# Kernel optimization log

Hardware: AMD Instinct MI355X
Metric: run time of the kernel (lower is better)

## Reference

```python
import jax, jax.numpy as jnp
import numpy as np

K = 4  # hard-coded in ParticleNet.__init__

# (fan_in, fan_out) for all linear layers
_DIMS = [(10, 32), (32, 64),        # edgeconv1 MLP (2*5 -> 32 -> 64)
         (128, 96), (96, 128),      # edgeconv2 MLP (2*64 -> 96 -> 128)
         (256, 192), (192, 256),    # edgeconv3 MLP (2*128 -> 192 -> 256)
         (453, 453), (453, 226), (226, 2)]  # output head (5+64+128+256=453)
_PNAMES = ['c1w1', 'c1w2', 'c2w1', 'c2w2', 'c3w1', 'c3w2', 'ow1', 'ow2', 'ow3']


def setup_inputs() -> dict:
    key = jax.random.key(0)
    ks = jax.random.split(key, 2 + len(_DIMS))
    inp = {
        'coords': jax.random.normal(ks[0], (1024, 128, 2), dtype=jnp.float32),
        'features': jax.random.normal(ks[1], (1024, 128, 5), dtype=jnp.float32),
    }
    for i, (name, (fi, fo)) in enumerate(zip(_PNAMES, _DIMS)):
        inp[name] = jax.random.normal(ks[2 + i], (fi, fo), dtype=jnp.float32) / np.sqrt(fi)
        inp[name.replace('w', 'b')] = jnp.zeros((fo,), dtype=jnp.float32)
    return inp


def _knn_idx(x, k):
    # x: [B,N,C] -> idx of k nearest neighbors (excluding self): [B,N,k]
    x2 = jnp.sum(x * x, axis=-1)                              # [B,N]
    d = x2[:, :, None] + x2[:, None, :] - 2.0 * jnp.einsum('bnc,bmc->bnm', x, x)
    d = d + jnp.eye(x.shape[1], dtype=x.dtype) * 1e9          # no self-loops
    _, idx = jax.lax.top_k(-d, k)
    return idx


def _edgeconv(x, idx, w1, b1, w2, b2):
    # EdgeConv: message = MLP([x_i, x_j - x_i]), mean-aggregated over k neighbors
    xj = jax.vmap(lambda xb, ib: xb[ib])(x, idx)              # [B,N,k,C]
    xi = jnp.broadcast_to(x[:, :, None, :], xj.shape)
    h = jnp.concatenate([xi, xj - xi], axis=-1)               # [B,N,k,2C]
    h = jax.nn.elu(h @ w1 + b1)
    h = jax.nn.elu(h @ w2 + b2)
    return jnp.mean(h, axis=2)                                # [B,N,out]


def reference(coords, features, c1w1, c1b1, c1w2, c1b2, c2w1, c2b1, c2w2, c2b2,
              c3w1, c3b1, c3w2, c3b2, ow1, ob1, ow2, ob2, ow3, ob3):
    idx1 = _knn_idx(coords, K)
    out1 = _edgeconv(features, idx1, c1w1, c1b1, c1w2, c1b2)  # [B,N,64]
    idx2 = _knn_idx(out1, K)
    out2 = _edgeconv(out1, idx2, c2w1, c2b1, c2w2, c2b2)      # [B,N,128]
    idx3 = _knn_idx(out2, K)
    out3 = _edgeconv(out2, idx3, c3w1, c3b1, c3w2, c3b2)      # [B,N,256]
    h = jnp.concatenate([features, out1, out2, out3], axis=-1)  # [B,N,453]
    h = jax.nn.elu(h @ ow1 + ob1)
    h = jax.nn.elu(h @ ow2 + ob2)
    return h @ ow3 + ob3                                      # [B,N,2]
```

## Files before the change

### kernel.cpp

```cpp
#include <hip/hip_runtime.h>
#include <cstdint>
#include <cstddef>


#define NB 1024
#define NPT 128

typedef __attribute__((ext_vector_type(8))) short short8;
typedef __attribute__((ext_vector_type(4))) float floatx4;
typedef __attribute__((ext_vector_type(4))) unsigned int uint4v;

__device__ __forceinline__ float elu_f(float x) { return x > 0.0f ? x : expm1f(x); }

__device__ __forceinline__ unsigned short f2bf(float f) {
  unsigned u = __builtin_bit_cast(unsigned, f);
  unsigned r = u + 0x7FFFu + ((u >> 16) & 1u);
  return (unsigned short)(r >> 16);
}
__device__ __forceinline__ float bf2f(unsigned short h) {
  unsigned u = ((unsigned)h) << 16;
  return __builtin_bit_cast(float, u);
}

template<int C>
__global__ __launch_bounds__(128) void knn_kernel(const float* __restrict__ x,
                                                  int* __restrict__ idx) {
  __shared__ __align__(16) float xs[NPT][C + 4];
  __shared__ float x2s[NPT];
  __shared__ double x2d[NPT];
  const int b = blockIdx.x, t = threadIdx.x;
  const float* xb = x + (size_t)b * NPT * C;
  for (int e = t; e < NPT * C; e += 128) xs[e / C][e % C] = xb[e];
  __syncthreads();
  float xi[C];
  float s2 = 0.0f;
  double s2d = 0.0;
#pragma unroll
  for (int c = 0; c < C; ++c) {
    xi[c] = xs[t][c];
    s2 += xi[c] * xi[c];
    s2d += (double)xi[c] * (double)xi[c];
  }
  x2s[t] = s2;
  x2d[t] = s2d;
  __syncthreads();
  float bd0 = 1e30f, bd1 = 1e30f, bd2 = 1e30f, bd3 = 1e30f, bd4 = 1e30f, bd5 = 1e30f;
  int bi0 = 0, bi1 = 0, bi2 = 0, bi3 = 0, bi4 = 0, bi5 = 0;
  for (int j = 0; j < NPT; ++j) {
    if (j == t) continue;
    float dot = 0.0f;
#pragma unroll
    for (int c = 0; c < C; ++c) dot += xi[c] * xs[j][c];
    float d = s2 + x2s[j] - 2.0f * dot;
    if (d < bd5) {
      bd5 = d; bi5 = j;
      if (bd5 < bd4) {
        float td = bd4; bd4 = bd5; bd5 = td; int ti = bi4; bi4 = bi5; bi5 = ti;
        if (bd4 < bd3) {
          td = bd3; bd3 = bd4; bd4 = td; ti = bi3; bi3 = bi4; bi4 = ti;
          if (bd3 < bd2) {
            td = bd2; bd2 = bd3; bd3 = td; ti = bi2; bi2 = bi3; bi3 = ti;
            if (bd2 < bd1) {
              td = bd1; bd1 = bd2; bd2 = td; ti = bi1; bi1 = bi2; bi2 = ti;
              if (bd1 < bd0) {
                td = bd0; bd0 = bd1; bd1 = td; ti = bi0; bi0 = bi1; bi1 = ti;
              }
            }
          }
        }
      }
    }
  }
  auto refine = [&](int j) -> double {
    double dot = 0.0;
#pragma unroll
    for (int c = 0; c < C; ++c) dot += (double)xi[c] * (double)xs[j][c];
    return s2d + x2d[j] - 2.0 * dot;
  };
  double e0 = refine(bi0), e1 = refine(bi1), e2 = refine(bi2);
  double e3 = refine(bi3), e4 = refine(bi4), e5 = refine(bi5);
#define CSWP(da, ia, db, ib)                                            \
  if ((da > db) || (da == db && ia > ib)) {                             \
    double _td = da; da = db; db = _td; int _ti = ia; ia = ib; ib = _ti; }
  CSWP(e0, bi0, e1, bi1) CSWP(e1, bi1, e2, bi2) CSWP(e2, bi2, e3, bi3)
  CSWP(e3, bi3, e4, bi4) CSWP(e4, bi4, e5, bi5)
  CSWP(e0, bi0, e1, bi1) CSWP(e1, bi1, e2, bi2) CSWP(e2, bi2, e3, bi3)
  CSWP(e3, bi3, e4, bi4)
  CSWP(e0, bi0, e1, bi1) CSWP(e1, bi1, e2, bi2) CSWP(e2, bi2, e3, bi3)
  CSWP(e0, bi0, e1, bi1) CSWP(e1, bi1, e2, bi2)
  CSWP(e0, bi0, e1, bi1)
#undef CSWP
  int* ib = idx + ((size_t)b * NPT + t) * 4;
  ib[0] = bi0; ib[1] = bi1; ib[2] = bi2; ib[3] = bi3;
}

template<int C>
__global__ __launch_bounds__(512) void knn512_kernel(const float* __restrict__ x,
                                                     int* __restrict__ idx) {
  constexpr int CQ = C / 4;
  constexpr int QS = CQ + 4;
  __shared__ __align__(16) float xs[NPT][4 * QS];
  __shared__ float x2s[NPT];
  __shared__ double x2d[NPT];
  const int b = blockIdx.x, t = threadIdx.x;
  const float* xb = x + (size_t)b * NPT * C;
  for (int e = t; e < NPT * C; e += 512) {
    int r = e / C, c = e % C;
    xs[r][(c / CQ) * QS + (c % CQ)] = xb[e];
  }
  __syncthreads();
  const int p = t >> 2, q = t & 3;
  float xi[CQ];
  float s2 = 0.f;
  double s2d = 0.0;
#pragma unroll
  for (int c = 0; c < CQ; ++c) {
    xi[c] = xs[p][q * QS + c];
    s2 += xi[c] * xi[c];
    s2d += (double)xi[c] * (double)xi[c];
  }
  s2 += __shfl_xor(s2, 1);  s2 += __shfl_xor(s2, 2);
  s2d += __shfl_xor(s2d, 1); s2d += __shfl_xor(s2d, 2);
  if (q == 0) { x2s[p] = s2; x2d[p] = s2d; }
  __syncthreads();
  float bd0 = 1e30f, bd1 = 1e30f, bd2 = 1e30f, bd3 = 1e30f, bd4 = 1e30f, bd5 = 1e30f;
  int bi0 = 0, bi1 = 0, bi2 = 0, bi3 = 0, bi4 = 0, bi5 = 0;
  for (int j = 0; j < NPT; ++j) {
    if (j == p) continue;
    const float4* xr = reinterpret_cast<const float4*>(&xs[j][q * QS]);
    float part0 = 0.f, part1 = 0.f, part2 = 0.f, part3 = 0.f;
#pragma unroll
    for (int c4 = 0; c4 < CQ / 4; ++c4) {
      float4 v = xr[c4];
      float s = xi[4 * c4 + 0] * v.x + xi[4 * c4 + 1] * v.y +
                xi[4 * c4 + 2] * v.z + xi[4 * c4 + 3] * v.w;
      if ((c4 & 3) == 0) part0 += s;
      else if ((c4 & 3) == 1) part1 += s;
      else if ((c4 & 3) == 2) part2 += s;
      else part3 += s;
    }
    float dot = (part0 + part1) + (part2 + part3);
    dot += __shfl_xor(dot, 1);
    dot += __shfl_xor(dot, 2);
    float d = s2 + x2s[j] - 2.0f * dot;
    if (d < bd5) {
      bd5 = d; bi5 = j;
      if (bd5 < bd4) {
        float td = bd4; bd4 = bd5; bd5 = td; int ti = bi4; bi4 = bi5; bi5 = ti;
        if (bd4 < bd3) {
          td = bd3; bd3 = bd4; bd4 = td; ti = bi3; bi3 = bi4; bi4 = ti;
          if (bd3 < bd2) {
            td = bd2; bd2 = bd3; bd3 = td; ti = bi2; bi2 = bi3; bi3 = ti;
            if (bd2 < bd1) {
              td = bd1; bd1 = bd2; bd2 = td; ti = bi1; bi1 = bi2; bi2 = ti;
              if (bd1 < bd0) {
                td = bd0; bd0 = bd1; bd1 = td; ti = bi0; bi0 = bi1; bi1 = ti;
              }
            }
          }
        }
      }
    }
  }
  auto refine = [&](int j) -> double {
    double dot = 0.0;
#pragma unroll
    for (int c = 0; c < CQ; ++c) dot += (double)xi[c] * (double)xs[j][q * QS + c];
    dot += __shfl_xor(dot, 1);
    dot += __shfl_xor(dot, 2);
    return s2d + x2d[j] - 2.0 * dot;
  };
  double e0 = refine(bi0), e1 = refine(bi1), e2 = refine(bi2);
  double e3 = refine(bi3), e4 = refine(bi4), e5 = refine(bi5);
#define CSWP(da, ia, db, ib)                                            \
  if ((da > db) || (da == db && ia > ib)) {                             \
    double _td = da; da = db; db = _td; int _ti = ia; ia = ib; ib = _ti; }
  CSWP(e0, bi0, e1, bi1) CSWP(e1, bi1, e2, bi2) CSWP(e2, bi2, e3, bi3)
  CSWP(e3, bi3, e4, bi4) CSWP(e4, bi4, e5, bi5)
  CSWP(e0, bi0, e1, bi1) CSWP(e1, bi1, e2, bi2) CSWP(e2, bi2, e3, bi3)
  CSWP(e3, bi3, e4, bi4)
  CSWP(e0, bi0, e1, bi1) CSWP(e1, bi1, e2, bi2) CSWP(e2, bi2, e3, bi3)
  CSWP(e0, bi0, e1, bi1) CSWP(e1, bi1, e2, bi2)
  CSWP(e0, bi0, e1, bi1)
#undef CSWP
  if (q == 0) {
    int* ib = idx + ((size_t)b * NPT + p) * 4;
    ib[0] = bi0; ib[1] = bi1; ib[2] = bi2; ib[3] = bi3;
  }
}

__global__ __launch_bounds__(256) void ec1_kernel(
    const float* __restrict__ feat, const int* __restrict__ idx,
    const float* __restrict__ w1, const float* __restrict__ b1,
    const float* __restrict__ w2, const float* __restrict__ b2,
    float* __restrict__ out) {
  __shared__ __align__(16) float fs[NPT][6];
  __shared__ __align__(16) float w1s[10][32];
  __shared__ __align__(16) float w2s[32][68];
  __shared__ float hs[256][33];
  __shared__ float b1s[32], b2s[64];
  const int z = blockIdx.x, t = threadIdx.x;
  const int b = z >> 1, hh = z & 1;
  const float* fb = feat + (size_t)b * NPT * 5;
  for (int e = t; e < NPT * 5; e += 256) fs[e / 5][e % 5] = fb[e];
  for (int e = t; e < 320; e += 256) w1s[e / 32][e % 32] = w1[e];
  for (int e = t; e < 2048; e += 256) w2s[e >> 6][e & 63] = w2[e];
  if (t < 32) b1s[t] = b1[t];
  if (t >= 192) b2s[t - 192] = b2[t - 192];
  __syncthreads();
  {
    const int p = hh * 64 + (t >> 2);
    const int j = idx[(size_t)b * 512 + p * 4 + (t & 3)];
    float h[32];
#pragma unroll
    for (int o = 0; o < 32; ++o) h[o] = b1s[o];
#pragma unroll
    for (int c = 0; c < 10; ++c) {
      float in_c = (c < 5) ? fs[p][c] : (fs[j][c - 5] - fs[p][c - 5]);
      const float4* wr = reinterpret_cast<const float4*>(&w1s[c][0]);
#pragma unroll
      for (int o4 = 0; o4 < 8; ++o4) {
        float4 w = wr[o4];
        h[4 * o4 + 0] += in_c * w.x; h[4 * o4 + 1] += in_c * w.y;
        h[4 * o4 + 2] += in_c * w.z; h[4 * o4 + 3] += in_c * w.w;
      }
    }
#pragma unroll
    for (int o = 0; o < 32; ++o) hs[t][o] = elu_f(h[o]);
  }
  __syncthreads();
  {
    const int g = t >> 2, q = t & 3;
    const int o0 = q * 16;
    float acc[4][16];
#pragma unroll
    for (int m = 0; m < 16; ++m) {
      float bv = b2s[o0 + m];
#pragma unroll
      for (int i = 0; i < 4; ++i) acc[i][m] = bv;
    }
    for (int k = 0; k < 32; ++k) {
      float hk0 = hs[g * 4 + 0][k];
      float hk1 = hs[g * 4 + 1][k];
      float hk2 = hs[g * 4 + 2][k];
      float hk3 = hs[g * 4 + 3][k];
      const float4* wr = reinterpret_cast<const float4*>(&w2s[k][o0]);
#pragma unroll
      for (int m4 = 0; m4 < 4; ++m4) {
        float4 w = wr[m4];
        acc[0][4 * m4 + 0] += hk0 * w.x; acc[0][4 * m4 + 1] += hk0 * w.y;
        acc[0][4 * m4 + 2] += hk0 * w.z; acc[0][4 * m4 + 3] += hk0 * w.w;
        acc[1][4 * m4 + 0] += hk1 * w.x; acc[1][4 * m4 + 1] += hk1 * w.y;
        acc[1][4 * m4 + 2] += hk1 * w.z; acc[1][4 * m4 + 3] += hk1 * w.w;
        acc[2][4 * m4 + 0] += hk2 * w.x; acc[2][4 * m4 + 1] += hk2 * w.y;
        acc[2][4 * m4 + 2] += hk2 * w.z; acc[2][4 * m4 + 3] += hk2 * w.w;
        acc[3][4 * m4 + 0] += hk3 * w.x; acc[3][4 * m4 + 1] += hk3 * w.y;
        acc[3][4 * m4 + 2] += hk3 * w.z; acc[3][4 * m4 + 3] += hk3 * w.w;
      }
    }
    float* ob = out + ((size_t)b * NPT + hh * 64 + g) * 64 + o0;
#pragma unroll
    for (int m4 = 0; m4 < 4; ++m4) {
      float4 v;
      float* vp = &v.x;
#pragma unroll
      for (int s = 0; s < 4; ++s) {
        int m = 4 * m4 + s;
        vp[s] = 0.25f * (elu_f(acc[0][m]) + elu_f(acc[1][m]) +
                         elu_f(acc[2][m]) + elu_f(acc[3][m]));
      }
      *reinterpret_cast<float4*>(&ob[4 * m4]) = v;
    }
  }
}

__global__ __launch_bounds__(512, 2) void ec2a_kernel(
    const float* __restrict__ x, const int* __restrict__ idx,
    const float* __restrict__ w1, const float* __restrict__ b1,
    float* __restrict__ H) {
  __shared__ __align__(16) float xs[NPT][68];
  __shared__ __align__(16) float w1s[128][100];
  __shared__ float b1s[96];
  const int b = blockIdx.x, t = threadIdx.x;
  const float* xb = x + (size_t)b * NPT * 64;
  for (int e = t; e < NPT * 64; e += 512) xs[e >> 6][e & 63] = xb[e];
  for (int e = t; e < 128 * 96; e += 512) w1s[e / 96][e % 96] = w1[e];
  if (t < 96) b1s[t] = b1[t];
  __syncthreads();
  const int pb = t >> 2, part = t & 3;
  const int n0 = part * 24;
  int jn[4];
#pragma unroll
  for (int i = 0; i < 4; ++i) jn[i] = idx[(size_t)b * 512 + pb * 4 + i];
  float acc[4][24];
#pragma unroll
  for (int m = 0; m < 24; ++m) {
    float bv = b1s[n0 + m];
#pragma unroll
    for (int i = 0; i < 4; ++i) acc[i][m] = bv;
  }
  for (int c = 0; c < 64; ++c) {
    float in_c = xs[pb][c];
    const float4* wr = reinterpret_cast<const float4*>(&w1s[c][n0]);
#pragma unroll
    for (int q4 = 0; q4 < 6; ++q4) {
      float4 wv = wr[q4];
#pragma unroll
      for (int i = 0; i < 4; ++i) {
        acc[i][4 * q4 + 0] += in_c * wv.x;
        acc[i][4 * q4 + 1] += in_c * wv.y;
        acc[i][4 * q4 + 2] += in_c * wv.z;
        acc[i][4 * q4 + 3] += in_c * wv.w;
      }
    }
  }
  for (int c = 0; c < 64; ++c) {
    float xic = xs[pb][c];
    float in0 = xs[jn[0]][c] - xic;
    float in1 = xs[jn[1]][c] - xic;
    float in2 = xs[jn[2]][c] - xic;
    float in3 = xs[jn[3]][c] - xic;
    const float4* wr = reinterpret_cast<const float4*>(&w1s[64 + c][n0]);
#pragma unroll
    for (int q4 = 0; q4 < 6; ++q4) {
      float4 wv = wr[q4];
      acc[0][4 * q4 + 0] += in0 * wv.x; acc[0][4 * q4 + 1] += in0 * wv.y;
      acc[0][4 * q4 + 2] += in0 * wv.z; acc[0][4 * q4 + 3] += in0 * wv.w;
      acc[1][4 * q4 + 0] += in1 * wv.x; acc[1][4 * q4 + 1] += in1 * wv.y;
      acc[1][4 * q4 + 2] += in1 * wv.z; acc[1][4 * q4 + 3] += in1 * wv.w;
      acc[2][4 * q4 + 0] += in2 * wv.x; acc[2][4 * q4 + 1] += in2 * wv.y;
      acc[2][4 * q4 + 2] += in2 * wv.z; acc[2][4 * q4 + 3] += in2 * wv.w;
      acc[3][4 * q4 + 0] += in3 * wv.x; acc[3][4 * q4 + 1] += in3 * wv.y;
      acc[3][4 * q4 + 2] += in3 * wv.z; acc[3][4 * q4 + 3] += in3 * wv.w;
    }
  }
#pragma unroll
  for (int i = 0; i < 4; ++i) {
    float* hrow = H + ((size_t)b * 512 + pb * 4 + i) * 96 + n0;
#pragma unroll
    for (int q4 = 0; q4 < 6; ++q4) {
      float4 v = {elu_f(acc[i][4 * q4 + 0]), elu_f(acc[i][4 * q4 + 1]),
                  elu_f(acc[i][4 * q4 + 2]), elu_f(acc[i][4 * q4 + 3])};
      *reinterpret_cast<float4*>(&hrow[4 * q4]) = v;
    }
  }
}

__global__ __launch_bounds__(512, 2) void ec2b_kernel(
    const float* __restrict__ H, const float* __restrict__ w2,
    const float* __restrict__ b2, float* __restrict__ out) {
  __shared__ __align__(16) float hsT[96][260];
  __shared__ float w2s[96][132];
  __shared__ float b2s[128];
  const int z = blockIdx.x, t = threadIdx.x;
  const int bc = z >> 1, hh = z & 1;
  const float* Hb = H + ((size_t)bc * 512 + hh * 256) * 96;
  for (int i = t; i < 256 * 96; i += 512) hsT[i % 96][i / 96] = Hb[i];
  for (int i = t; i < 96 * 128; i += 512) w2s[i >> 7][i & 127] = w2[i];
  if (t < 128) b2s[t] = b2[t];
  __syncthreads();
  const int g = t >> 3, oq = t & 7;
  float acc[4][16];
#pragma unroll
  for (int m = 0; m < 16; ++m) {
    float bv = b2s[oq + 8 * m];
#pragma unroll
    for (int i = 0; i < 4; ++i) acc[i][m] = bv;
  }
  for (int k = 0; k < 96; ++k) {
    float4 hv = *reinterpret_cast<const float4*>(&hsT[k][4 * g]);
#pragma unroll
    for (int m = 0; m < 16; ++m) {
      float wv = w2s[k][oq + 8 * m];
      acc[0][m] += hv.x * wv;
      acc[1][m] += hv.y * wv;
      acc[2][m] += hv.z * wv;
      acc[3][m] += hv.w * wv;
    }
  }
  float* orow = out + ((size_t)bc * NPT + hh * 64 + g) * 128;
#pragma unroll
  for (int m = 0; m < 16; ++m) {
    float s = elu_f(acc[0][m]) + elu_f(acc[1][m]) +
              elu_f(acc[2][m]) + elu_f(acc[3][m]);
    orow[oq + 8 * m] = 0.25f * s;
  }
}

__global__ __launch_bounds__(512, 2) void ec3a_kernel(
    const float* __restrict__ x, const int* __restrict__ idx,
    const float* __restrict__ w1, const float* __restrict__ b1,
    unsigned short* __restrict__ h1) {
  __shared__ unsigned short Xb[128][136];
  __shared__ unsigned short W1t[192][264];
  __shared__ float b1s[192];
  __shared__ unsigned short stg[8][16][40];
  const int b = blockIdx.x, t = threadIdx.x;
  const float* xb = x + (size_t)b * NPT * 128;
  for (int e = t; e < NPT * 128; e += 512) Xb[e >> 7][e & 127] = f2bf(xb[e]);
  for (int e = t; e < 256 * 192; e += 512) {
    int k = e / 192, n = e % 192;
    W1t[n][k] = f2bf(w1[e]);
  }
  if (t < 192) b1s[t] = b1[t];
  __syncthreads();
  const int w = t >> 6, l = t & 63;
  const int lr = l & 15, lq = l >> 4;
  for (int mt = 0; mt < 4; ++mt) {
    const int m = (w * 4 + mt) * 16;
    const int e = m + lr;
    const int p = e >> 2;
    const int jp = idx[(size_t)b * 512 + e];
    short8 A[8];
#pragma unroll
    for (int kk = 0; kk < 4; ++kk) {
      int k0 = kk * 32 + lq * 8;
      A[kk] = *reinterpret_cast<const short8*>(&Xb[p][k0]);
    }
#pragma unroll
    for (int kk = 0; kk < 4; ++kk) {
      int k0 = kk * 32 + lq * 8;
      short8 aj = *reinterpret_cast<const short8*>(&Xb[jp][k0]);
      short8 ai = *reinterpret_cast<const short8*>(&Xb[p][k0]);
      short8 d;
#pragma unroll
      for (int q = 0; q < 8; ++q)
        d[q] = (short)f2bf(bf2f((unsigned short)aj[q]) - bf2f((unsigned short)ai[q]));
      A[4 + kk] = d;
    }
    floatx4 acc[12];
#pragma unroll
    for (int n = 0; n < 12; ++n) acc[n] = (floatx4){0.f, 0.f, 0.f, 0.f};
#pragma unroll
    for (int n = 0; n < 12; ++n) {
#pragma unroll
      for (int kk = 0; kk < 8; ++kk) {
        short8 Bf = *reinterpret_cast<const short8*>(&W1t[n * 16 + lr][kk * 32 + lq * 8]);
        acc[n] = __builtin_amdgcn_mfma_f32_16x16x32_bf16(A[kk], Bf, acc[n], 0, 0, 0);
      }
    }
#pragma unroll
    for (int pr = 0; pr < 6; ++pr) {
      float bv0 = b1s[pr * 32 + lr];
      float bv1 = b1s[pr * 32 + 16 + lr];
#pragma unroll
      for (int i = 0; i < 4; ++i) {
        stg[w][lq * 4 + i][lr]      = f2bf(elu_f(acc[2 * pr][i] + bv0));
        stg[w][lq * 4 + i][16 + lr] = f2bf(elu_f(acc[2 * pr + 1][i] + bv1));
      }
      asm volatile("s_waitcnt lgkmcnt(0)" ::: "memory");
      const unsigned short* src = &stg[w][l >> 2][(l & 3) * 8];
      uint4v vv = *reinterpret_cast<const uint4v*>(src);
      size_t dst = ((size_t)b * 512 + m + (l >> 2)) * 192 + pr * 32 + (l & 3) * 8;
      *reinterpret_cast<uint4v*>(&h1[dst]) = vv;
      asm volatile("s_waitcnt lgkmcnt(0)" ::: "memory");
    }
  }
}

__global__ __launch_bounds__(512, 2) void ec3b_kernel(
    const unsigned short* __restrict__ h1,
    const float* __restrict__ w2, const float* __restrict__ b2,
    unsigned short* __restrict__ out3) {
  __shared__ unsigned short W2t[256][200];
  __shared__ float b2s[256];
  const int b = blockIdx.x, t = threadIdx.x;
  for (int e = t; e < 192 * 256; e += 512) {
    int k = e >> 8, n = e & 255;
    W2t[n][k] = f2bf(w2[e]);
  }
  if (t < 256) b2s[t] = b2[t];
  __syncthreads();
  const int w = t >> 6, l = t & 63;
  const int lr = l & 15, lq = l >> 4;
  for (int mt = 0; mt < 4; ++mt) {
    const int m = (w * 4 + mt) * 16;
    floatx4 acc[16];
#pragma unroll
    for (int n = 0; n < 16; ++n) acc[n] = (floatx4){0.f, 0.f, 0.f, 0.f};
    const unsigned short* arow = h1 + ((size_t)b * 512 + m + lr) * 192;
#pragma unroll
    for (int kk = 0; kk < 6; ++kk) {
      short8 Af = *reinterpret_cast<const short8*>(&arow[kk * 32 + lq * 8]);
#pragma unroll
      for (int n = 0; n < 16; ++n) {
        short8 Bf = *reinterpret_cast<const short8*>(&W2t[n * 16 + lr][kk * 32 + lq * 8]);
        acc[n] = __builtin_amdgcn_mfma_f32_16x16x32_bf16(Af, Bf, acc[n], 0, 0, 0);
      }
    }
    unsigned short* orow = out3 + ((size_t)b * NPT + (m >> 2) + lq) * 256;
#pragma unroll
    for (int n = 0; n < 16; ++n) {
      float bv = b2s[n * 16 + lr];
      float s = 0.f;
#pragma unroll
      for (int i = 0; i < 4; ++i) s += elu_f(acc[n][i] + bv);
      orow[n * 16 + lr] = f2bf(0.25f * s);
    }
  }
}

__global__ __launch_bounds__(256) void head_prep_kernel(
    const float* __restrict__ w1, const float* __restrict__ w2,
    unsigned short* __restrict__ w1p, unsigned short* __restrict__ w2p) {
  int i = blockIdx.x * 256 + threadIdx.x;
  if (i < 512 * 480) {
    int n = i / 480, kp = i % 480;
    int ko = (kp < 5) ? kp : kp - 3;
    bool ok = ((kp < 5) || (kp >= 8 && kp < 456)) && (n < 453);
    w1p[i] = ok ? f2bf(w1[(size_t)ko * 453 + n]) : (unsigned short)0;
  } else {
    int j = i - 512 * 480;
    if (j < 256 * 480) {
      int n = j / 480, kp = j % 480;
      bool ok = (kp < 453) && (n < 226);
      w2p[j] = ok ? f2bf(w2[(size_t)kp * 226 + n]) : (unsigned short)0;
    }
  }
}

#define HSTR 488
#define TPSS 72
__global__ __launch_bounds__(256, 2) void head_mfma_kernel(
    const float* __restrict__ feat, const float* __restrict__ o1,
    const float* __restrict__ o2, const unsigned short* __restrict__ o3,
    const unsigned short* __restrict__ w1p, const float* __restrict__ b1,
    const unsigned short* __restrict__ w2p, const float* __restrict__ b2,
    const float* __restrict__ w3, const float* __restrict__ b3,
    float* __restrict__ out) {
  __shared__ unsigned short uA[64 * HSTR];
  __shared__ __align__(16) unsigned short tps[4][16][TPSS];
  __shared__ float b1s[512], b2s[256], w3s[512];
  const int t = threadIdx.x;
  const size_t base = (size_t)blockIdx.x * 64;

  for (int e = t; e < 64 * 8; e += 256) {
    int r = e >> 3, c = e & 7;
    uA[r * HSTR + c] = (c < 5) ? f2bf(feat[(base + r) * 5 + c]) : 0;
  }
  for (int e = t; e < 64 * 64; e += 256) {
    int r = e >> 6, c = e & 63;
    uA[r * HSTR + 8 + c] = f2bf(o1[(base + r) * 64 + c]);
  }
  for (int e = t; e < 64 * 128; e += 256) {
    int r = e >> 7, c = e & 127;
    uA[r * HSTR + 72 + c] = f2bf(o2[(base + r) * 128 + c]);
  }
  for (int e = t; e < 64 * 256; e += 256) {
    int r = e >> 8, c = e & 255;
    uA[r * HSTR + 200 + c] = o3[(base + r) * 256 + c];
  }
  for (int e = t; e < 64 * 32; e += 256) {
    int r = e >> 5, c = e & 31;
    uA[r * HSTR + 456 + c] = 0;
  }
  for (int i = t; i < 512; i += 256) b1s[i] = (i < 453) ? b1[i] : 0.f;
  if (t < 256) b2s[t] = (t < 226) ? b2[t] : 0.f;
  for (int i = t; i < 512; i += 256) w3s[i] = (i < 452) ? w3[i] : 0.f;
  __syncthreads();

  const int w = t >> 6, l = t & 63;
  const int lr = l & 15, lq = l >> 4;
  const int tr = t >> 2, tc = t & 3;

  short8 Af[15];
#pragma unroll
  for (int kk = 0; kk < 15; ++kk)
    Af[kk] = *reinterpret_cast<const short8*>(
        &uA[(w * 16 + lr) * HSTR + kk * 32 + lq * 8]);
  __syncthreads();

  uint4v v[15];
#define WLOAD(SRC, CH)                                                   \
  {                                                                      \
    _Pragma("unroll")                                                    \
    for (int i = 0; i < 15; ++i)                                         \
      v[i] = *reinterpret_cast<const uint4v*>(                           \
          &SRC[((size_t)((CH) * 64 + tr)) * 480 + (tc + 4 * i) * 8]);    \
  }
#define WWRITE()                                                         \
  {                                                                      \
    _Pragma("unroll")                                                    \
    for (int i = 0; i < 15; ++i)                                         \
      *reinterpret_cast<uint4v*>(&uA[tr * HSTR + (tc + 4 * i) * 8]) = v[i]; \
  }

  WLOAD(w1p, 0)
  WWRITE()
  __syncthreads();

  short8 Af2[15];
#pragma unroll
  for (int ch = 0; ch < 8; ++ch) {
    if (ch < 7) WLOAD(w1p, ch + 1)
    else       WLOAD(w2p, 0)
    floatx4 a0 = {0.f, 0.f, 0.f, 0.f}, a1 = {0.f, 0.f, 0.f, 0.f};
    floatx4 a2 = {0.f, 0.f, 0.f, 0.f}, a3 = {0.f, 0.f, 0.f, 0.f};
#pragma unroll
    for (int kk = 0; kk < 15; ++kk) {
      int ko = kk * 32 + lq * 8;
      short8 B0 = *reinterpret_cast<const short8*>(&uA[(lr)*HSTR + ko]);
      short8 B1 = *reinterpret_cast<const short8*>(&uA[(16 + lr) * HSTR + ko]);
      short8 B2 = *reinterpret_cast<const short8*>(&uA[(32 + lr) * HSTR + ko]);
      short8 B3 = *reinterpret_cast<const short8*>(&uA[(48 + lr) * HSTR + ko]);
      a0 = __builtin_amdgcn_mfma_f32_16x16x32_bf16(Af[kk], B0, a0, 0, 0, 0);
      a1 = __builtin_amdgcn_mfma_f32_16x16x32_bf16(Af[kk], B1, a1, 0, 0, 0);
      a2 = __builtin_amdgcn_mfma_f32_16x16x32_bf16(Af[kk], B2, a2, 0, 0, 0);
      a3 = __builtin_amdgcn_mfma_f32_16x16x32_bf16(Af[kk], B3, a3, 0, 0, 0);
    }
    {
      floatx4 aj[4] = {a0, a1, a2, a3};
#pragma unroll
      for (int jx = 0; jx < 4; ++jx) {
        int c = ch * 64 + jx * 16 + lr;
        float bb = b1s[c];
#pragma unroll
        for (int i = 0; i < 4; ++i)
          tps[w][lq * 4 + i][jx * 16 + lr] = f2bf(elu_f(aj[jx][i] + bb));
      }
    }
    asm volatile("s_waitcnt lgkmcnt(0)" ::: "memory");
    Af2[2 * ch] = *reinterpret_cast<const short8*>(&tps[w][lr][lq * 8]);
    if (ch < 7)
      Af2[2 * ch + 1] = *reinterpret_cast<const short8*>(&tps[w][lr][32 + lq * 8]);
    asm volatile("s_waitcnt lgkmcnt(0)" ::: "memory");
    __syncthreads();
    WWRITE()
    __syncthreads();
  }

  float p0[4] = {0.f, 0.f, 0.f, 0.f}, p1[4] = {0.f, 0.f, 0.f, 0.f};
#pragma unroll
  for (int ch = 0; ch < 4; ++ch) {
    if (ch < 3) WLOAD(w2p, ch + 1)
    floatx4 a0 = {0.f, 0.f, 0.f, 0.f}, a1 = {0.f, 0.f, 0.f, 0.f};
    floatx4 a2 = {0.f, 0.f, 0.f, 0.f}, a3 = {0.f, 0.f, 0.f, 0.f};
#pragma unroll
    for (int kk = 0; kk < 15; ++kk) {
      int ko = kk * 32 + lq * 8;
      short8 B0 = *reinterpret_cast<const short8*>(&uA[(lr)*HSTR + ko]);
      short8 B1 = *reinterpret_cast<const short8*>(&uA[(16 + lr) * HSTR + ko]);
      short8 B2 = *reinterpret_cast<const short8*>(&uA[(32 + lr) * HSTR + ko]);
      short8 B3 = *reinterpret_cast<const short8*>(&uA[(48 + lr) * HSTR + ko]);
      a0 = __builtin_amdgcn_mfma_f32_16x16x32_bf16(Af2[kk], B0, a0, 0, 0, 0);
      a1 = __builtin_amdgcn_mfma_f32_16x16x32_bf16(Af2[kk], B1, a1, 0, 0, 0);
      a2 = __builtin_amdgcn_mfma_f32_16x16x32_bf16(Af2[kk], B2, a2, 0, 0, 0);
      a3 = __builtin_amdgcn_mfma_f32_16x16x32_bf16(Af2[kk], B3, a3, 0, 0, 0);
    }
    {
      floatx4 aj[4] = {a0, a1, a2, a3};
#pragma unroll
      for (int jx = 0; jx < 4; ++jx) {
        int c = ch * 64 + jx * 16 + lr;
        float bb = b2s[c];
        float wa = w3s[2 * c], wb = w3s[2 * c + 1];
#pragma unroll
        for (int i = 0; i < 4; ++i) {
          float h = (c < 226) ? elu_f(aj[jx][i] + bb) : 0.f;
          p0[i] += h * wa;
          p1[i] += h * wb;
        }
      }
    }
    if (ch < 3) {
      __syncthreads();
      WWRITE()
      __syncthreads();
    }
  }

#pragma unroll
  for (int i = 0; i < 4; ++i) {
    float a = p0[i], bvv = p1[i];
#pragma unroll
    for (int m = 1; m < 16; m <<= 1) {
      a += __shfl_xor(a, m);
      bvv += __shfl_xor(bvv, m);
    }
    if (lr == 0) {
      size_t row = base + w * 16 + lq * 4 + i;
      float2 vv = {a + b3[0], bvv + b3[1]};
      *reinterpret_cast<float2*>(&out[row * 2]) = vv;
    }
  }
#undef WLOAD
#undef WWRITE
}

extern "C" void kernel_launch(void* const* d_in, const int* in_sizes, int n_in,
                              void* d_out, int out_size, void* d_ws, size_t ws_size,
                              hipStream_t stream) {
  const float* coords = (const float*)d_in[0];
  const float* feat   = (const float*)d_in[1];
  const float* c1w1 = (const float*)d_in[2];  const float* c1b1 = (const float*)d_in[3];
  const float* c1w2 = (const float*)d_in[4];  const float* c1b2 = (const float*)d_in[5];
  const float* c2w1 = (const float*)d_in[6];  const float* c2b1 = (const float*)d_in[7];
  const float* c2w2 = (const float*)d_in[8];  const float* c2b2 = (const float*)d_in[9];
  const float* c3w1 = (const float*)d_in[10]; const float* c3b1 = (const float*)d_in[11];
  const float* c3w2 = (const float*)d_in[12]; const float* c3b2 = (const float*)d_in[13];
  const float* ow1  = (const float*)d_in[14]; const float* ob1  = (const float*)d_in[15];
  const float* ow2  = (const float*)d_in[16]; const float* ob2  = (const float*)d_in[17];
  const float* ow3  = (const float*)d_in[18]; const float* ob3  = (const float*)d_in[19];
  float* out = (float*)d_out;

  char* ws = (char*)d_ws;
  float* out1 = (float*)(ws);
  float* out2 = (float*)(ws + (32ull << 20));
  unsigned short* out3b = (unsigned short*)(ws + (96ull << 20));
  int* idx = (int*)(ws + (160ull << 20));
  float* Hbuf = (float*)(ws + (162ull << 20));
  unsigned short* h1 = (unsigned short*)(ws + (162ull << 20));
  unsigned short* w1p = (unsigned short*)(ws + (212ull << 20));
  unsigned short* w2p = (unsigned short*)(ws + (213ull << 20));

  head_prep_kernel<<<1440, 256, 0, stream>>>(ow1, ow2, w1p, w2p);
  knn_kernel<2><<<NB, 128, 0, stream>>>(coords, idx);
  ec1_kernel<<<2 * NB, 256, 0, stream>>>(feat, idx, c1w1, c1b1, c1w2, c1b2, out1);
  knn512_kernel<64><<<NB, 512, 0, stream>>>(out1, idx);
  for (int c = 0; c < 4; ++c) {
    ec2a_kernel<<<256, 512, 0, stream>>>(out1 + (size_t)c * 256 * NPT * 64,
                                         idx + (size_t)c * 256 * 512,
                                         c2w1, c2b1, Hbuf);
    ec2b_kernel<<<512, 512, 0, stream>>>(Hbuf, c2w2, c2b2,
                                         out2 + (size_t)c * 256 * NPT * 128);
  }
  knn512_kernel<128><<<NB, 512, 0, stream>>>(out2, idx);
  for (int c = 0; c < 4; ++c) {
    ec3a_kernel<<<256, 512, 0, stream>>>(out2 + (size_t)c * 256 * NPT * 128,
                                         idx + (size_t)c * 256 * 512,
                                         c3w1, c3b1, h1);
    ec3b_kernel<<<256, 512, 0, stream>>>(h1, c3w2, c3b2,
                                         out3b + (size_t)c * 256 * NPT * 256);
  }
  head_mfma_kernel<<<2048, 256, 0, stream>>>(feat, out1, out2, out3b,
                                             w1p, ob1, w2p, ob2, ow3, ob3, out);
}
```

Measured before the change: 2.002 ms.

## Pretranspose ec3 weights once, load head inputs directly, enlarge ec2 chunks

The ec3 layer weights are now converted to bf16 and transposed once in a combined prep kernel. The ec3a/ec3b blocks then copy them into shared memory with vectorized 16-byte loads, instead of each block doing a strided scalar transpose and conversion. The head kernel now loads its A fragments straight from global memory into registers, skipping shared-memory staging and two barriers. ec2 runs in 2 chunks of 512 batches rather than 4, using a larger Hbuf region that aliases the out3 buffer. This aliasing is safe only if ec2 finishes before ec3 writes out3. The change adds workspace relayout and loads the head's global data with less coalescing.

```diff
diff --git a/kernel.cpp b/kernel.cpp
--- a/kernel.cpp
+++ b/kernel.cpp
@@ -389,18 +389,19 @@
 
 __global__ __launch_bounds__(512, 2) void ec3a_kernel(
     const float* __restrict__ x, const int* __restrict__ idx,
-    const float* __restrict__ w1, const float* __restrict__ b1,
+    const unsigned short* __restrict__ w1t3g, const float* __restrict__ b1,
     unsigned short* __restrict__ h1) {
   __shared__ unsigned short Xb[128][136];
-  __shared__ unsigned short W1t[192][264];
+  __shared__ __align__(16) unsigned short W1t[192][264];
   __shared__ float b1s[192];
   __shared__ unsigned short stg[8][16][40];
   const int b = blockIdx.x, t = threadIdx.x;
   const float* xb = x + (size_t)b * NPT * 128;
   for (int e = t; e < NPT * 128; e += 512) Xb[e >> 7][e & 127] = f2bf(xb[e]);
-  for (int e = t; e < 256 * 192; e += 512) {
-    int k = e / 192, n = e % 192;
-    W1t[n][k] = f2bf(w1[e]);
+  {
+    const uint4v* src = reinterpret_cast<const uint4v*>(w1t3g);
+    uint4v* dst = reinterpret_cast<uint4v*>(&W1t[0][0]);
+    for (int i = t; i < 192 * 264 / 8; i += 512) dst[i] = src[i];
   }
   if (t < 192) b1s[t] = b1[t];
   __syncthreads();
@@ -460,14 +461,15 @@
 
 __global__ __launch_bounds__(512, 2) void ec3b_kernel(
     const unsigned short* __restrict__ h1,
-    const float* __restrict__ w2, const float* __restrict__ b2,
+    const unsigned short* __restrict__ w2t3g, const float* __restrict__ b2,
     unsigned short* __restrict__ out3) {
-  __shared__ unsigned short W2t[256][200];
+  __shared__ __align__(16) unsigned short W2t[256][200];
   __shared__ float b2s[256];
   const int b = blockIdx.x, t = threadIdx.x;
-  for (int e = t; e < 192 * 256; e += 512) {
-    int k = e >> 8, n = e & 255;
-    W2t[n][k] = f2bf(w2[e]);
+  {
+    const uint4v* src = reinterpret_cast<const uint4v*>(w2t3g);
+    uint4v* dst = reinterpret_cast<uint4v*>(&W2t[0][0]);
+    for (int i = t; i < 256 * 200 / 8; i += 512) dst[i] = src[i];
   }
   if (t < 256) b2s[t] = b2[t];
   __syncthreads();
@@ -500,21 +502,31 @@
   }
 }
 
-__global__ __launch_bounds__(256) void head_prep_kernel(
-    const float* __restrict__ w1, const float* __restrict__ w2,
-    unsigned short* __restrict__ w1p, unsigned short* __restrict__ w2p) {
+__global__ __launch_bounds__(256) void prep_kernel(
+    const float* __restrict__ hw1, const float* __restrict__ hw2,
+    const float* __restrict__ c3w1, const float* __restrict__ c3w2,
+    unsigned short* __restrict__ w1p, unsigned short* __restrict__ w2p,
+    unsigned short* __restrict__ w1t3g, unsigned short* __restrict__ w2t3g) {
   int i = blockIdx.x * 256 + threadIdx.x;
   if (i < 512 * 480) {
     int n = i / 480, kp = i % 480;
     int ko = (kp < 5) ? kp : kp - 3;
     bool ok = ((kp < 5) || (kp >= 8 && kp < 456)) && (n < 453);
-    w1p[i] = ok ? f2bf(w1[(size_t)ko * 453 + n]) : (unsigned short)0;
+    w1p[i] = ok ? f2bf(hw1[(size_t)ko * 453 + n]) : (unsigned short)0;
+  } else if (i < 512 * 480 + 256 * 480) {
+    int j = i - 512 * 480;
+    int n = j / 480, kp = j % 480;
+    bool ok = (kp < 453) && (n < 226);
+    w2p[j] = ok ? f2bf(hw2[(size_t)kp * 226 + n]) : (unsigned short)0;
+  } else if (i < 512 * 480 + 256 * 480 + 192 * 264) {
+    int m = i - (512 * 480 + 256 * 480);
+    int n = m / 264, k = m % 264;
+    w1t3g[m] = (k < 256) ? f2bf(c3w1[(size_t)k * 192 + n]) : (unsigned short)0;
   } else {
-    int j = i - 512 * 480;
-    if (j < 256 * 480) {
-      int n = j / 480, kp = j % 480;
-      bool ok = (kp < 453) && (n < 226);
-      w2p[j] = ok ? f2bf(w2[(size_t)kp * 226 + n]) : (unsigned short)0;
+    int m = i - (512 * 480 + 256 * 480 + 192 * 264);
+    if (m < 256 * 200) {
+      int n = m / 200, k = m % 200;
+      w2t3g[m] = (k < 192) ? f2bf(c3w2[(size_t)k * 256 + n]) : (unsigned short)0;
     }
   }
 }
@@ -534,41 +546,40 @@
   const int t = threadIdx.x;
   const size_t base = (size_t)blockIdx.x * 64;
 
-  for (int e = t; e < 64 * 8; e += 256) {
-    int r = e >> 3, c = e & 7;
-    uA[r * HSTR + c] = (c < 5) ? f2bf(feat[(base + r) * 5 + c]) : 0;
-  }
-  for (int e = t; e < 64 * 64; e += 256) {
-    int r = e >> 6, c = e & 63;
-    uA[r * HSTR + 8 + c] = f2bf(o1[(base + r) * 64 + c]);
-  }
-  for (int e = t; e < 64 * 128; e += 256) {
-    int r = e >> 7, c = e & 127;
-    uA[r * HSTR + 72 + c] = f2bf(o2[(base + r) * 128 + c]);
-  }
-  for (int e = t; e < 64 * 256; e += 256) {
-    int r = e >> 8, c = e & 255;
-    uA[r * HSTR + 200 + c] = o3[(base + r) * 256 + c];
-  }
-  for (int e = t; e < 64 * 32; e += 256) {
-    int r = e >> 5, c = e & 31;
-    uA[r * HSTR + 456 + c] = 0;
-  }
   for (int i = t; i < 512; i += 256) b1s[i] = (i < 453) ? b1[i] : 0.f;
   if (t < 256) b2s[t] = (t < 226) ? b2[t] : 0.f;
   for (int i = t; i < 512; i += 256) w3s[i] = (i < 452) ? w3[i] : 0.f;
-  __syncthreads();
 
   const int w = t >> 6, l = t & 63;
   const int lr = l & 15, lq = l >> 4;
   const int tr = t >> 2, tc = t & 3;
+  const size_t grow = base + w * 16 + lr;
 
   short8 Af[15];
 #pragma unroll
-  for (int kk = 0; kk < 15; ++kk)
-    Af[kk] = *reinterpret_cast<const short8*>(
-        &uA[(w * 16 + lr) * HSTR + kk * 32 + lq * 8]);
-  __syncthreads();
+  for (int kk = 0; kk < 15; ++kk) {
+    const int kbase = kk * 32 + lq * 8;
+    short8 r;
+    if (kbase >= 456) {
+#pragma unroll
+      for (int q = 0; q < 8; ++q) r[q] = 0;
+    } else if (kbase >= 200) {
+      r = *reinterpret_cast<const short8*>(&o3[grow * 256 + (kbase - 200)]);
+    } else if (kbase >= 72) {
+      const float* s = &o2[grow * 128 + (kbase - 72)];
+#pragma unroll
+      for (int q = 0; q < 8; ++q) r[q] = (short)f2bf(s[q]);
+    } else if (kbase >= 8) {
+      const float* s = &o1[grow * 64 + (kbase - 8)];
+#pragma unroll
+      for (int q = 0; q < 8; ++q) r[q] = (short)f2bf(s[q]);
+    } else {
+      const float* s = &feat[grow * 5];
+#pragma unroll
+      for (int q = 0; q < 8; ++q) r[q] = (q < 5) ? (short)f2bf(s[q]) : (short)0;
+    }
+    Af[kk] = r;
+  }
 
   uint4v v[15];
 #define WLOAD(SRC, CH)                                                   \
@@ -707,29 +718,32 @@
   float* out1 = (float*)(ws);
   float* out2 = (float*)(ws + (32ull << 20));
   unsigned short* out3b = (unsigned short*)(ws + (96ull << 20));
-  int* idx = (int*)(ws + (160ull << 20));
-  float* Hbuf = (float*)(ws + (162ull << 20));
+  float* Hbuf2 = (float*)(ws + (96ull << 20));
   unsigned short* h1 = (unsigned short*)(ws + (162ull << 20));
   unsigned short* w1p = (unsigned short*)(ws + (212ull << 20));
-  unsigned short* w2p = (unsigned short*)(ws + (213ull << 20));
-
-  head_prep_kernel<<<1440, 256, 0, stream>>>(ow1, ow2, w1p, w2p);
+  unsigned short* w2p = (unsigned short*)(ws + (212ull << 20) + (512ull << 10));
+  unsigned short* w1t3g = (unsigned short*)(ws + (213ull << 20));
+  unsigned short* w2t3g = (unsigned short*)(ws + (213ull << 20) + (256ull << 10));
+  int* idx = (int*)(ws + (214ull << 20));
+
+  prep_kernel<<<1838, 256, 0, stream>>>(ow1, ow2, c3w1, c3w2,
+                                        w1p, w2p, w1t3g, w2t3g);
   knn_kernel<2><<<NB, 128, 0, stream>>>(coords, idx);
   ec1_kernel<<<2 * NB, 256, 0, stream>>>(feat, idx, c1w1, c1b1, c1w2, c1b2, out1);
   knn512_kernel<64><<<NB, 512, 0, stream>>>(out1, idx);
-  for (int c = 0; c < 4; ++c) {
-    ec2a_kernel<<<256, 512, 0, stream>>>(out1 + (size_t)c * 256 * NPT * 64,
-                                         idx + (size_t)c * 256 * 512,
-                                         c2w1, c2b1, Hbuf);
-    ec2b_kernel<<<512, 512, 0, stream>>>(Hbuf, c2w2, c2b2,
-                                         out2 + (size_t)c * 256 * NPT * 128);
+  for (int c = 0; c < 2; ++c) {
+    ec2a_kernel<<<512, 512, 0, stream>>>(out1 + (size_t)c * 512 * NPT * 64,
+                                         idx + (size_t)c * 512 * 512,
+                                         c2w1, c2b1, Hbuf2);
+    ec2b_kernel<<<1024, 512, 0, stream>>>(Hbuf2, c2w2, c2b2,
+                                          out2 + (size_t)c * 512 * NPT * 128);
   }
   knn512_kernel<128><<<NB, 512, 0, stream>>>(out2, idx);
   for (int c = 0; c < 4; ++c) {
     ec3a_kernel<<<256, 512, 0, stream>>>(out2 + (size_t)c * 256 * NPT * 128,
                                          idx + (size_t)c * 256 * 512,
-                                         c3w1, c3b1, h1);
-    ec3b_kernel<<<256, 512, 0, stream>>>(h1, c3w2, c3b2,
+                                         w1t3g, c3b1, h1);
+    ec3b_kernel<<<256, 512, 0, stream>>>(h1, w2t3g, c3b2,
                                          out3b + (size_t)c * 256 * NPT * 256);
   }
   head_mfma_kernel<<<2048, 256, 0, stream>>>(feat, out1, out2, out3b,
```

Result: no change. 1.981 ms (-1.0%).
